# Kernel tuning notes

Measured on AMD Instinct MI355X. Metric: run time of the kernel, lower is better.

Reference implementation:

```python
import jax, jax.numpy as jnp
import numpy as np

# dims: B batch, CIN/COUT channels, K kernel, H/W spatial, S stride, P padding
B, CIN, COUT, K, H, W, S, P = 8, 16, 64, 3, 32, 32, 1, 1
ALPHA, R, N_EKV, VT, VD = 0.05625, 0.1, 1.5, 0.025, 0.1


def setup_inputs() -> dict:
    key = jax.random.key(0)
    k1, k2 = jax.random.split(key)
    x = jax.random.normal(k1, (B, CIN, H, W), dtype=jnp.float32)
    # torch init: uniform_(theta, 1.0, 8.0)
    theta = jax.random.uniform(k2, (COUT, CIN * K * K), dtype=jnp.float32, minval=1.0, maxval=8.0)
    scale = jnp.array(1.0, dtype=jnp.float32)
    return {"x": x, "theta": theta, "scale": scale}


def _unfold(x, k, s, p):
    # torch.nn.Unfold: patches flattened channel-major as (C, kh, kw)
    b, c, h, w = x.shape
    ho = (h + 2 * p - k) // s + 1
    wo = (w + 2 * p - k) // s + 1
    xp = jnp.pad(x, ((0, 0), (0, 0), (p, p), (p, p)))
    patches = jnp.stack(
        [xp[:, :, i:i + ho * s:s, j:j + wo * s:s] for i in range(k) for j in range(k)],
        axis=2,
    )  # (B, C, K*K, Ho, Wo)
    return patches.reshape(b, c * k * k, ho * wo), ho, wo


def _log1p_exp_stable_sq(a):
    # clamp to [-50, 20] then softplus; squared (EKV f)
    a = jnp.clip(a, -50.0, 20.0)
    sp = jnp.log1p(jnp.exp(a))
    return sp * sp


def reference(x, theta, scale):
    theta = jnp.clip(theta, 1.0, 8.0)  # mirrors theta.data.clamp_(1, 8)
    vg, ho, wo = _unfold(x, K, S, P)          # (B, Cin*K^2, L)
    vg = vg[:, None, :, :]                    # (B, 1, Cin*K^2, L)
    vth = theta[None, :, :, None]             # (1, Cout, Cin*K^2, 1)
    denom = 2.0 * N_EKV * VT
    term1 = _log1p_exp_stable_sq((vg - vth) / denom)
    term2 = _log1p_exp_stable_sq((vg - vth - VD) / denom)
    currents = jnp.clip(ALPHA * (term1 - term2), 0.0, None)
    i_k = jnp.sum(currents, axis=2)           # reduce over Cin*K^2 -> (B, Cout, L)
    v_out = i_k * R * scale
    return v_out.reshape(x.shape[0], COUT, ho, wo)
```

## Files before the change

### kernel.cpp

```cpp
#include <hip/hip_runtime.h>
#include <hip/hip_bf16.h>

#define BB 8
#define CIN 16
#define COUT 64
#define HH 32
#define WW 32
#define PH 34
#define PW 34
#define PPLANE (PH * PW)

#define INV_DENOM_LOG2E 19.235933878519388f
#define K2E 0.26359713811472845f
#define B_HI 28.85390081777927f
#define WIN_C 0.46f
#define WIN_HW 1.16f
#define OUT_CONST (0.4804530139182014f * 0.05625f * 0.1f)

#define EXP2F(x) __builtin_amdgcn_exp2f(x)
#define LOG2F(x) __builtin_amdgcn_logf(x)

__global__ __launch_bounds__(256) void pad_x_kernel(const float* __restrict__ x,
                                                    float* __restrict__ xp) {
    int idx = blockIdx.x * 256 + threadIdx.x;
    int c = idx / PPLANE;
    int r = idx - c * PPLANE;
    int y = r / PW;
    int xc = r - y * PW;
    float v = 0.0f;
    if (y >= 1 && y <= HH && xc >= 1 && xc <= WW) {
        v = x[c * (HH * WW) + (y - 1) * WW + (xc - 1)];
    }
    xp[idx] = v;
}

__device__ __forceinline__ void ekv_eval(float d, float& acc) {
    float b1 = d * INV_DENOM_LOG2E;
    float e1 = EXP2F(b1);
    float e2 = e1 * K2E;
    float l1 = fminf(LOG2F(1.0f + e1), B_HI);
    float l2 = fminf(LOG2F(1.0f + e2), B_HI);
    acc = fmaf(l1, l1, acc);
    acc = fmaf(-l2, l2, acc);
}

__device__ __forceinline__ void load9(const float* __restrict__ p, float* v) {
#pragma unroll
    for (int dy = 0; dy < 3; ++dy)
#pragma unroll
        for (int dx = 0; dx < 3; ++dx)
            v[dy * 3 + dx] = p[dy * PW + dx];
}

__device__ __forceinline__ void compute9(const float* v, const float* __restrict__ sth,
                                         float& acc) {
    float th[9];
#pragma unroll
    for (int j = 0; j < 9; ++j) th[j] = sth[j];
#pragma unroll
    for (int k = 0; k < 9; ++k) {
        float d = v[k] - th[k];
        if (__any(fabsf(d - WIN_C) < WIN_HW)) ekv_eval(d, acc);
    }
}

__global__ __launch_bounds__(256, 8) void ekv_kernel(const float* __restrict__ xp,
                                                     const float* __restrict__ theta,
                                                     const float* __restrict__ scale,
                                                     float* __restrict__ out) {
    int bid = blockIdx.x;
    int co = bid & 63;
    int tile = (bid >> 6) & 3;
    int b = bid >> 8;

    int t = threadIdx.x;
    int ow = t & 31;
    int oh = tile * 8 + (t >> 5);

    __shared__ __align__(16) float s_th[CIN * 12];
    if (t < CIN * 12) {
        int cin = t / 12;
        int j = t - cin * 12;
        float v = 0.0f;
        if (j < 9) {
            float th = theta[co * (CIN * 9) + cin * 9 + j];
            v = fminf(fmaxf(th, 1.0f), 8.0f);
        }
        s_th[t] = v;
    }
    __syncthreads();

    float acc = 0.0f;

    const float* p0 = xp + (size_t)b * (CIN * PPLANE) + oh * PW + ow;
    float va[9], vb[9];
    load9(p0, va);
#pragma unroll 1
    for (int cin = 0; cin < CIN; cin += 2) {
        load9(p0 + (cin + 1) * PPLANE, vb);
        compute9(va, s_th + cin * 12, acc);
        int nc = cin + 2 < CIN ? cin + 2 : CIN - 1;
        load9(p0 + nc * PPLANE, va);
        compute9(vb, s_th + (cin + 1) * 12, acc);
    }

    float sc = scale[0] * (OUT_CONST);
    out[(((size_t)b * COUT + co) * HH + oh) * WW + ow] = acc * sc;
}

extern "C" void kernel_launch(void* const* d_in, const int* in_sizes, int n_in,
                              void* d_out, int out_size, void* d_ws, size_t ws_size,
                              hipStream_t stream) {
    const float* x = (const float*)d_in[0];
    const float* theta = (const float*)d_in[1];
    const float* scale = (const float*)d_in[2];
    float* out = (float*)d_out;

    constexpr size_t PAD_ELEMS = (size_t)BB * CIN * PPLANE;
    constexpr size_t PAD_BYTES = (PAD_ELEMS + 4) * sizeof(float);

    float* xp = (float*)d_ws;
    (void)ws_size;
    pad_x_kernel<<<(int)(PAD_ELEMS / 256), 256, 0, stream>>>(x, xp);
    ekv_kernel<<<BB * 4 * COUT, 256, 0, stream>>>(xp, theta, scale, out);
    (void)PAD_BYTES;
}
```

Measured before the change: 75.71 us.

## Replace EKV transcendental evaluation with interpolated shared-memory lookup table

The per-element softplus-squared difference (exp plus two logs, skipped when a whole wave falls outside the active window) is replaced by a 2048-entry table of value and slope, indexed by the clamped difference and linearly interpolated. The table is built once per call in an extra block fused into the padding kernel. Each compute block copies it into 16 KB of LDS. The accumulator is split three ways to shorten the dependency chain. This trades transcendental math for LDS gathers, which can hit bank conflicts, plus a 16 KB table copy per block. It also gives up the wave-level skip of inactive elements and adds an interpolation error.

```diff
diff --git a/kernel.cpp b/kernel.cpp
--- a/kernel.cpp
+++ b/kernel.cpp
@@ -1,5 +1,4 @@
 #include <hip/hip_runtime.h>
-#include <hip/hip_bf16.h>
 
 #define BB 8
 #define CIN 16
@@ -10,38 +9,45 @@
 #define PW 34
 #define PPLANE (PH * PW)
 
-#define INV_DENOM_LOG2E 19.235933878519388f
-#define K2E 0.26359713811472845f
-#define B_HI 28.85390081777927f
-#define WIN_C 0.46f
-#define WIN_HW 1.16f
-#define OUT_CONST (0.4804530139182014f * 0.05625f * 0.1f)
+#define LUT_N 2048
+#define LUT_LO (-0.75f)
+#define LUT_STEP (2.4f / (float)LUT_N)
+#define LUT_INVSTEP ((float)LUT_N / 2.4f)
+#define LUT_BIAS 640.0f
+#define LUT_TMAX 2046.999f
+#define OUT_SCALE (0.05625f * 0.1f)
 
-#define EXP2F(x) __builtin_amdgcn_exp2f(x)
-#define LOG2F(x) __builtin_amdgcn_logf(x)
-
-__global__ __launch_bounds__(256) void pad_x_kernel(const float* __restrict__ x,
-                                                    float* __restrict__ xp) {
-    int idx = blockIdx.x * 256 + threadIdx.x;
-    int c = idx / PPLANE;
-    int r = idx - c * PPLANE;
-    int y = r / PW;
-    int xc = r - y * PW;
-    float v = 0.0f;
-    if (y >= 1 && y <= HH && xc >= 1 && xc <= WW) {
-        v = x[c * (HH * WW) + (y - 1) * WW + (xc - 1)];
-    }
-    xp[idx] = v;
+__device__ __forceinline__ float lut_f(float d) {
+    const float C = 13.333333f;
+    float a1 = fminf(fmaxf(d * C, -50.0f), 20.0f);
+    float a2 = fminf(fmaxf((d - 0.1f) * C, -50.0f), 20.0f);
+    float s1 = log1pf(expf(a1));
+    float s2 = log1pf(expf(a2));
+    return fmaxf(s1 * s1 - s2 * s2, 0.0f);
 }
 
-__device__ __forceinline__ void ekv_eval(float d, float& acc) {
-    float b1 = d * INV_DENOM_LOG2E;
-    float e1 = EXP2F(b1);
-    float e2 = e1 * K2E;
-    float l1 = fminf(LOG2F(1.0f + e1), B_HI);
-    float l2 = fminf(LOG2F(1.0f + e2), B_HI);
-    acc = fmaf(l1, l1, acc);
-    acc = fmaf(-l2, l2, acc);
+__global__ __launch_bounds__(256) void init_kernel(const float* __restrict__ x,
+                                                   float* __restrict__ xp,
+                                                   float2* __restrict__ lut_g) {
+    if (blockIdx.x < 578) {
+        int idx = blockIdx.x * 256 + threadIdx.x;
+        int c = idx / PPLANE;
+        int r = idx - c * PPLANE;
+        int y = r / PW;
+        int xc = r - y * PW;
+        float v = 0.0f;
+        if (y >= 1 && y <= HH && xc >= 1 && xc <= WW) {
+            v = x[c * (HH * WW) + (y - 1) * WW + (xc - 1)];
+        }
+        xp[idx] = v;
+    } else {
+        for (int i = threadIdx.x; i < LUT_N; i += 256) {
+            float d0 = LUT_LO + (float)i * LUT_STEP;
+            float v0 = lut_f(d0);
+            float v1 = lut_f(d0 + LUT_STEP);
+            lut_g[i] = make_float2(v0, v1 - v0);
+        }
+    }
 }
 
 __device__ __forceinline__ void load9(const float* __restrict__ p, float* v) {
@@ -53,18 +59,24 @@
 }
 
 __device__ __forceinline__ void compute9(const float* v, const float* __restrict__ sth,
-                                         float& acc) {
+                                         const float2* __restrict__ lut, float* acc) {
     float th[9];
 #pragma unroll
     for (int j = 0; j < 9; ++j) th[j] = sth[j];
 #pragma unroll
     for (int k = 0; k < 9; ++k) {
         float d = v[k] - th[k];
-        if (__any(fabsf(d - WIN_C) < WIN_HW)) ekv_eval(d, acc);
+        float t = fmaf(d, LUT_INVSTEP, LUT_BIAS);
+        t = fminf(fmaxf(t, 0.0f), LUT_TMAX);
+        int i = (int)t;
+        float fr = t - (float)i;
+        float2 e = lut[i];
+        acc[k % 3] += fmaf(fr, e.y, e.x);
     }
 }
 
 __global__ __launch_bounds__(256, 8) void ekv_kernel(const float* __restrict__ xp,
+                                                     const float2* __restrict__ lut_g,
                                                      const float* __restrict__ theta,
                                                      const float* __restrict__ scale,
                                                      float* __restrict__ out) {
@@ -77,7 +89,15 @@
     int ow = t & 31;
     int oh = tile * 8 + (t >> 5);
 
+    __shared__ __align__(16) float2 s_lut[LUT_N];
     __shared__ __align__(16) float s_th[CIN * 12];
+
+    {
+        const float4* g = (const float4*)lut_g;
+        float4* s = (float4*)s_lut;
+#pragma unroll
+        for (int i = 0; i < 4; ++i) s[t + i * 256] = g[t + i * 256];
+    }
     if (t < CIN * 12) {
         int cin = t / 12;
         int j = t - cin * 12;
@@ -90,7 +110,7 @@
     }
     __syncthreads();
 
-    float acc = 0.0f;
+    float acc[3] = {0.0f, 0.0f, 0.0f};
 
     const float* p0 = xp + (size_t)b * (CIN * PPLANE) + oh * PW + ow;
     float va[9], vb[9];
@@ -98,14 +118,15 @@
 #pragma unroll 1
     for (int cin = 0; cin < CIN; cin += 2) {
         load9(p0 + (cin + 1) * PPLANE, vb);
-        compute9(va, s_th + cin * 12, acc);
+        compute9(va, s_th + cin * 12, s_lut, acc);
         int nc = cin + 2 < CIN ? cin + 2 : CIN - 1;
         load9(p0 + nc * PPLANE, va);
-        compute9(vb, s_th + (cin + 1) * 12, acc);
+        compute9(vb, s_th + (cin + 1) * 12, s_lut, acc);
     }
 
-    float sc = scale[0] * (OUT_CONST);
-    out[(((size_t)b * COUT + co) * HH + oh) * WW + ow] = acc * sc;
+    float sc = scale[0] * (OUT_SCALE);
+    out[(((size_t)b * COUT + co) * HH + oh) * WW + ow] =
+        (acc[0] + acc[1] + acc[2]) * sc;
 }
 
 extern "C" void kernel_launch(void* const* d_in, const int* in_sizes, int n_in,
@@ -116,12 +137,10 @@
     const float* scale = (const float*)d_in[2];
     float* out = (float*)d_out;
 
-    constexpr size_t PAD_ELEMS = (size_t)BB * CIN * PPLANE;
-    constexpr size_t PAD_BYTES = (PAD_ELEMS + 4) * sizeof(float);
+    float2* lut_g = (float2*)d_ws;
+    float* xp = (float*)((char*)d_ws + LUT_N * sizeof(float2));
+    (void)ws_size;
 
-    float* xp = (float*)d_ws;
-    (void)ws_size;
-    pad_x_kernel<<<(int)(PAD_ELEMS / 256), 256, 0, stream>>>(x, xp);
-    ekv_kernel<<<BB * 4 * COUT, 256, 0, stream>>>(xp, theta, scale, out);
-    (void)PAD_BYTES;
+    init_kernel<<<579, 256, 0, stream>>>(x, xp, lut_g);
+    ekv_kernel<<<BB * 4 * COUT, 256, 0, stream>>>(xp, lut_g, theta, scale, out);
 }
```

New measurement: 87.37 us. 1.15x slower.
